# Kernel tuning notes

Measured on AMD Instinct MI355X. Metric: run time of the kernel, lower is better.

Reference implementation:

```python
import jax, jax.numpy as jnp
import numpy as np

K = 4
EPS = 1e-6
NEG_INF = -1e9


def _extract_patches(x, k):
    # x: [C, H, W] -> [P, C*k*k], P = (H-k+1)*(W-k+1), p = hp*Wp + wp
    C, H, W = x.shape
    Hp, Wp = H - k + 1, W - k + 1
    cols = jnp.stack([x[:, di:di + Hp, dj:dj + Wp]
                      for di in range(k) for dj in range(k)], axis=1)  # [C, k*k, Hp, Wp]
    return cols.reshape(C * k * k, Hp * Wp).T  # [P, C*k*k]


def setup_inputs() -> dict:
    key = jax.random.key(0)
    k1, k2, k3 = jax.random.split(key, 3)
    C, H, W = 32, 80, 80
    low = jax.random.normal(k1, (1, C, H, W), dtype=jnp.float32)
    high = jax.random.normal(k2, (1, C, H, W), dtype=jnp.float32)
    mask = jax.random.randint(k3, (H + 1, W + 1), 0, 2, dtype=jnp.int32)
    return {"low_level_features": low, "hight_level_features": high, "mask": mask}


def reference(low_level_features, hight_level_features, mask):
    k = K
    low = low_level_features[0]    # [C, H, W]
    high = hight_level_features[0]
    C, H, W = low.shape
    Hp, Wp = H - k + 1, W - k + 1
    P = Hp * Wp

    low_p = _extract_patches(low, k)    # [P, D], D = C*k*k (candidate patches)
    high_p = _extract_patches(high, k)  # [P, D] (query filters)
    norms = jnp.sqrt(jnp.sum(low_p * low_p, axis=1))  # torch.norm per patch, [P]

    # all-pairs cosine-distance scores: [P_query, P_candidate]
    scores = jnp.einsum('qd,pd->qp', high_p, low_p) / (norms + EPS)[None, :]
    # candidates where mask==1 (top-left of patch) are excluded (set to inf=-1e9)
    excl = (mask[:Hp, :Wp].reshape(-1) == 1)
    scores = jnp.where(excl[None, :], NEG_INF, scores)
    best = jnp.argmax(scores, axis=1)   # [P] best match per query patch

    # a query patch at (i,j) is processed only if its 4 mask corners are nonzero
    valid = ((mask[:Hp, :Wp] != 0) & (mask[:Hp, k:k + Wp] != 0) &
             (mask[k:k + Hp, :Wp] != 0) & (mask[k:k + Hp, k:k + Wp] != 0))
    validf = valid.astype(low.dtype).reshape(-1)  # [P]

    gathered = low_p[best] * validf[:, None]            # [P, D]
    g = gathered.reshape(Hp, Wp, C, k, k)               # per-query result patches
    vmap2d = validf.reshape(Hp, Wp)

    result = jnp.zeros_like(low)
    counts = jnp.zeros((H, W), low.dtype)
    for di in range(k):
        for dj in range(k):
            result = result.at[:, di:di + Hp, dj:dj + Wp].add(
                jnp.moveaxis(g[:, :, :, di, dj], -1, 0))
            counts = counts.at[di:di + Hp, dj:dj + Wp].add(vmap2d)

    out = result / (counts + EPS)[None, :, :]
    nz = counts != 0
    out = out * nz[None, :, :] + low * (~nz)[None, :, :]
    return out[None]  # [1, C, H, W]
```

## Files before the change

kernel.cpp:

```cpp
#include <hip/hip_runtime.h>
#include <hip/hip_bf16.h>

#define CC    32
#define HH    80
#define WW    80
#define HW    6400
#define HPQ   77
#define WPQ   77
#define PP    5929
#define DD    512
#define MSTR  81
#define NTILE 93
#define QTILES 372
#define NEGINF (-1e9f)

typedef __attribute__((ext_vector_type(4))) float f32x4;
typedef __attribute__((ext_vector_type(8))) short bf16x8;
typedef __attribute__((ext_vector_type(8))) unsigned short u16x8;

__device__ __forceinline__ void split_bf16(float v, unsigned short& hi, unsigned short& lo) {
    __hip_bfloat16 h = __float2bfloat16(v);
    float hf = __bfloat162float(h);
    __hip_bfloat16 lw = __float2bfloat16(v - hf);
    hi = *reinterpret_cast<unsigned short*>(&h);
    lo = *reinterpret_cast<unsigned short*>(&lw);
}

__global__ __launch_bounds__(256) void k_flags(const float* __restrict__ low,
                                               const int* __restrict__ mask,
                                               float* __restrict__ invn,
                                               int* __restrict__ excl,
                                               int* __restrict__ qslot,
                                               int* __restrict__ qlist,
                                               int* __restrict__ nvalid) {
    __shared__ float part[4][64];
    const int tid = threadIdx.x;
    const int pl = tid & 63;
    const int sl = tid >> 6;
    const int p = blockIdx.x * 64 + pl;

    float s = 0.f;
    if (p < PP) {
        int pi = p / WPQ, pj = p % WPQ;
        int base = pi * WW + pj;
        for (int c = sl * 8; c < sl * 8 + 8; ++c) {
            int b2 = c * HW + base;
#pragma unroll
            for (int di = 0; di < 4; ++di)
#pragma unroll
                for (int dj = 0; dj < 4; ++dj) {
                    float v = low[b2 + di * WW + dj];
                    s += v * v;
                }
        }
    }
    part[sl][pl] = s;
    __syncthreads();
    if (tid < 64 && p < PP) {
        float t = part[0][tid] + part[1][tid] + part[2][tid] + part[3][tid];
        invn[p] = 1.0f / (sqrtf(t) + 1e-6f);
        int pi = p / WPQ, pj = p % WPQ;
        int m00 = mask[pi * MSTR + pj];
        int m01 = mask[pi * MSTR + pj + 4];
        int m10 = mask[(pi + 4) * MSTR + pj];
        int m11 = mask[(pi + 4) * MSTR + pj + 4];
        excl[p] = (m00 == 1) ? 1 : 0;
        int v = (m00 != 0 && m01 != 0 && m10 != 0 && m11 != 0) ? 1 : 0;
        int slot = -1;
        if (v) {
            slot = atomicAdd(nvalid, 1);
            qlist[slot] = p;
        }
        qslot[p] = slot;
    }
}

__global__ __launch_bounds__(256) void k_pack(const float* __restrict__ low,
                                              const float* __restrict__ high,
                                              const float* __restrict__ invn,
                                              const int* __restrict__ qlist,
                                              const int* __restrict__ nvalid,
                                              unsigned short* __restrict__ Bhi,
                                              unsigned short* __restrict__ Blo,
                                              unsigned short* __restrict__ Ahi,
                                              unsigned short* __restrict__ Alo) {
    const int g = blockIdx.x;
    if (g < QTILES * 4) {
        int t = g * 256 + threadIdx.x;
        int l = t & 63;
        int s = (t >> 6) & 15;
        int u = t >> 10;
        int n = l & 15, quad = l >> 4;
        int p = u * 16 + n;
        int kbase = s * 32 + quad * 8;
        u16x8 vh, vl;
        if (p < PP) {
            float sc = invn[p];
            int pi = p / WPQ, pj = p % WPQ;
            int base = (kbase >> 4) * HW + pi * WW + pj;
#pragma unroll
            for (int j = 0; j < 8; ++j) {
                int kk = kbase + j;
                int di = (kk >> 2) & 3, dj = kk & 3;
                float v = low[base + di * WW + dj] * sc;
                unsigned short h, lo;
                split_bf16(v, h, lo);
                vh[j] = h; vl[j] = lo;
            }
        } else {
#pragma unroll
            for (int j = 0; j < 8; ++j) { vh[j] = 0; vl[j] = 0; }
        }
        int off = t * 8;
        *reinterpret_cast<u16x8*>(Bhi + off) = vh;
        *reinterpret_cast<u16x8*>(Blo + off) = vl;
    } else {
        int t = (g - QTILES * 4) * 256 + threadIdx.x;
        int nv = *nvalid;
        int l = t & 63;
        int s = (t >> 6) & 15;
        int u = t >> 10;
        if ((u >> 2) * 64 >= nv) return;
        int m = l & 15, quad = l >> 4;
        int slot = u * 16 + m;
        int kbase = s * 32 + quad * 8;
        u16x8 vh, vl;
        if (slot < nv) {
            int q = qlist[slot];
            int qi = q / WPQ, qj = q % WPQ;
            int base = (kbase >> 4) * HW + qi * WW + qj;
#pragma unroll
            for (int j = 0; j < 8; ++j) {
                int kk = kbase + j;
                int di = (kk >> 2) & 3, dj = kk & 3;
                float v = high[base + di * WW + dj];
                unsigned short h, lo;
                split_bf16(v, h, lo);
                vh[j] = h; vl[j] = lo;
            }
        } else {
#pragma unroll
            for (int j = 0; j < 8; ++j) { vh[j] = 0; vl[j] = 0; }
        }
        int off = t * 8;
        *reinterpret_cast<u16x8*>(Ahi + off) = vh;
        *reinterpret_cast<u16x8*>(Alo + off) = vl;
    }
}

__global__ __launch_bounds__(256) void k_score(const unsigned short* __restrict__ Ahi,
                                               const unsigned short* __restrict__ Alo,
                                               const unsigned short* __restrict__ Bhi,
                                               const unsigned short* __restrict__ Blo,
                                               const int* __restrict__ excl,
                                               const int* __restrict__ nvalid,
                                               unsigned long long* __restrict__ bestpk) {
    const int nv = *nvalid;
    const int w = threadIdx.x >> 6;
    const int l = threadIdx.x & 63;
    const int pblk = blockIdx.x * 4 + w;
    const int n = l & 15, quad = l >> 4;
    const int bbase = pblk * 4 * 8192 + l * 8;

    int gpv[4]; bool exv[4];
#pragma unroll
    for (int pt = 0; pt < 4; ++pt) {
        gpv[pt] = pblk * 64 + pt * 16 + n;
        exv[pt] = (gpv[pt] < PP) ? (excl[gpv[pt]] != 0) : true;
    }

    for (int qblk = blockIdx.y; qblk * 64 < nv; qblk += 12) {
        f32x4 acc[4][4];
#pragma unroll
        for (int qt = 0; qt < 4; ++qt)
#pragma unroll
            for (int pt = 0; pt < 4; ++pt) acc[qt][pt] = (f32x4){0.f, 0.f, 0.f, 0.f};

        const int abase = qblk * 4 * 8192 + l * 8;
#pragma unroll 2
        for (int s = 0; s < 16; ++s) {
            bf16x8 ah[4], al[4];
#pragma unroll
            for (int qt = 0; qt < 4; ++qt) {
                ah[qt] = *reinterpret_cast<const bf16x8*>(Ahi + abase + qt * 8192 + s * 512);
                al[qt] = *reinterpret_cast<const bf16x8*>(Alo + abase + qt * 8192 + s * 512);
            }
#pragma unroll
            for (int pt = 0; pt < 4; ++pt) {
                bf16x8 bh = *reinterpret_cast<const bf16x8*>(Bhi + bbase + pt * 8192 + s * 512);
                bf16x8 bl = *reinterpret_cast<const bf16x8*>(Blo + bbase + pt * 8192 + s * 512);
#pragma unroll
                for (int qt = 0; qt < 4; ++qt) {
                    acc[qt][pt] = __builtin_amdgcn_mfma_f32_16x16x32_bf16(ah[qt], bh, acc[qt][pt], 0, 0, 0);
                    acc[qt][pt] = __builtin_amdgcn_mfma_f32_16x16x32_bf16(ah[qt], bl, acc[qt][pt], 0, 0, 0);
                    acc[qt][pt] = __builtin_amdgcn_mfma_f32_16x16x32_bf16(al[qt], bh, acc[qt][pt], 0, 0, 0);
                }
            }
        }

#pragma unroll
        for (int qt = 0; qt < 4; ++qt) {
            float bs[4]; int bi[4];
#pragma unroll
            for (int r = 0; r < 4; ++r) { bs[r] = -3.4e38f; bi[r] = 0x7fffffff; }
#pragma unroll
            for (int pt = 0; pt < 4; ++pt) {
                if (gpv[pt] < PP) {
#pragma unroll
                    for (int r = 0; r < 4; ++r) {
                        float sv = exv[pt] ? NEGINF : acc[qt][pt][r];
                        if (sv > bs[r]) { bs[r] = sv; bi[r] = gpv[pt]; }
                    }
                }
            }
#pragma unroll
            for (int off = 1; off <= 8; off <<= 1) {
#pragma unroll
                for (int r = 0; r < 4; ++r) {
                    float s2 = __shfl_xor(bs[r], off, 64);
                    int   i2 = __shfl_xor(bi[r], off, 64);
                    if (s2 > bs[r] || (s2 == bs[r] && i2 < bi[r])) { bs[r] = s2; bi[r] = i2; }
                }
            }
            if (n == 0) {
#pragma unroll
                for (int r = 0; r < 4; ++r) {
                    if (bi[r] != 0x7fffffff) {
                        unsigned ub = __float_as_uint(bs[r]);
                        unsigned mo = (ub & 0x80000000u) ? ~ub : (ub | 0x80000000u);
                        unsigned long long pk =
                            ((unsigned long long)mo << 32) | (unsigned)(~bi[r]);
                        int slot = (qblk * 4 + qt) * 16 + quad * 4 + r;
                        atomicMax(bestpk + slot, pk);
                    }
                }
            }
        }
    }
}

__global__ __launch_bounds__(256) void k_out(const float* __restrict__ low,
                                             const int* __restrict__ qslot,
                                             const unsigned long long* __restrict__ bestpk,
                                             float* __restrict__ out) {
    __shared__ int scnt[64];
    __shared__ int soff[64][17];
    const int tid = threadIdx.x;
    const int pixb = blockIdx.x * 64;
    if (tid < 64) {
        int pix = pixb + tid;
        int i = pix / WW, j = pix % WW;
        int nn = 0;
#pragma unroll
        for (int di = 0; di < 4; ++di) {
            int qi = i - di;
            if (qi < 0 || qi >= HPQ) continue;
#pragma unroll
            for (int dj = 0; dj < 4; ++dj) {
                int qj = j - dj;
                if (qj < 0 || qj >= WPQ) continue;
                int sl = qslot[qi * WPQ + qj];
                if (sl >= 0) {
                    int b = (int)(~(unsigned)bestpk[sl]);
                    soff[tid][nn++] = (b / WPQ + di) * WW + (b % WPQ + dj);
                }
            }
        }
        scnt[tid] = nn;
    }
    __syncthreads();
    const int pl = tid & 63, cg = tid >> 6;
    const int nn = scnt[pl];
    const int pix = pixb + pl;
    const float inv = 1.0f / ((float)nn + 1e-6f);
#pragma unroll
    for (int k = 0; k < 8; ++k) {
        int c = cg * 8 + k;
        int base = c * HW;
        float a;
        if (nn > 0) {
            a = 0.f;
            for (int t2 = 0; t2 < nn; ++t2) a += low[base + soff[pl][t2]];
            a *= inv;
        } else {
            a = low[base + pix];
        }
        out[base + pix] = a;
    }
}

extern "C" void kernel_launch(void* const* d_in, const int* in_sizes, int n_in,
                              void* d_out, int out_size, void* d_ws, size_t ws_size,
                              hipStream_t stream) {
    const float* low  = (const float*)d_in[0];
    const float* high = (const float*)d_in[1];
    const int*   mask = (const int*)d_in[2];
    float* out = (float*)d_out;

    char* ws = (char*)d_ws;
    int* nvalid = (int*)ws;
    unsigned long long* bestpk = (unsigned long long*)(ws + 64);
    int*   qlist = (int*)(ws + 49216);
    int*   qslot = (int*)(ws + 73024);
    float* invn  = (float*)(ws + 96832);
    int*   excl  = (int*)(ws + 120640);
    unsigned short* Ahi = (unsigned short*)(ws + 144448);
    unsigned short* Alo = (unsigned short*)(ws + 6239296);
    unsigned short* Bhi = (unsigned short*)(ws + 12334144);
    unsigned short* Blo = (unsigned short*)(ws + 18625600);

    hipMemsetAsync(ws, 0, 49216, stream);
    hipLaunchKernelGGL(k_flags, dim3(NTILE), dim3(256), 0, stream,
                       low, mask, invn, excl, qslot, qlist, nvalid);
    hipLaunchKernelGGL(k_pack, dim3(QTILES * 8), dim3(256), 0, stream,
                       low, high, invn, qlist, nvalid, Bhi, Blo, Ahi, Alo);
    hipLaunchKernelGGL(k_score, dim3(24, 12), dim3(256), 0, stream,
                       Ahi, Alo, Bhi, Blo, excl, nvalid, bestpk);
    hipLaunchKernelGGL(k_out, dim3(100), dim3(256), 0, stream,
                       low, qslot, bestpk, out);
}
```

Measured before the change: 114.2 us.

## Fuse flag and pack kernels, apply norm scale in epilogue, retile score grid

Merges the flag/norm kernel with the packing kernel into one launch. The candidate norm scaling moves out of B packing and into the score epilogue, and each flag block packs its own valid query patches straight into their atomically assigned slots. The score kernel is retiled so each wave handles one query tile against a block's 64 candidates, with a grid of 93x12 instead of 24x12. This removes a launch and a dependency bubble and increases parallelism in scoring. In exchange, each wave reuses B fragments less, and the scale is applied after the hi/lo split rather than before it, which slightly changes the rounding.

```diff
diff --git a/kernel.cpp b/kernel.cpp
--- a/kernel.cpp
+++ b/kernel.cpp
@@ -26,67 +26,22 @@
     lo = *reinterpret_cast<unsigned short*>(&lw);
 }
 
-__global__ __launch_bounds__(256) void k_flags(const float* __restrict__ low,
-                                               const int* __restrict__ mask,
-                                               float* __restrict__ invn,
-                                               int* __restrict__ excl,
-                                               int* __restrict__ qslot,
-                                               int* __restrict__ qlist,
-                                               int* __restrict__ nvalid) {
-    __shared__ float part[4][64];
-    const int tid = threadIdx.x;
-    const int pl = tid & 63;
-    const int sl = tid >> 6;
-    const int p = blockIdx.x * 64 + pl;
-
-    float s = 0.f;
-    if (p < PP) {
-        int pi = p / WPQ, pj = p % WPQ;
-        int base = pi * WW + pj;
-        for (int c = sl * 8; c < sl * 8 + 8; ++c) {
-            int b2 = c * HW + base;
-#pragma unroll
-            for (int di = 0; di < 4; ++di)
-#pragma unroll
-                for (int dj = 0; dj < 4; ++dj) {
-                    float v = low[b2 + di * WW + dj];
-                    s += v * v;
-                }
-        }
-    }
-    part[sl][pl] = s;
-    __syncthreads();
-    if (tid < 64 && p < PP) {
-        float t = part[0][tid] + part[1][tid] + part[2][tid] + part[3][tid];
-        invn[p] = 1.0f / (sqrtf(t) + 1e-6f);
-        int pi = p / WPQ, pj = p % WPQ;
-        int m00 = mask[pi * MSTR + pj];
-        int m01 = mask[pi * MSTR + pj + 4];
-        int m10 = mask[(pi + 4) * MSTR + pj];
-        int m11 = mask[(pi + 4) * MSTR + pj + 4];
-        excl[p] = (m00 == 1) ? 1 : 0;
-        int v = (m00 != 0 && m01 != 0 && m10 != 0 && m11 != 0) ? 1 : 0;
-        int slot = -1;
-        if (v) {
-            slot = atomicAdd(nvalid, 1);
-            qlist[slot] = p;
-        }
-        qslot[p] = slot;
-    }
-}
-
-__global__ __launch_bounds__(256) void k_pack(const float* __restrict__ low,
+__global__ __launch_bounds__(256) void k_main(const float* __restrict__ low,
                                               const float* __restrict__ high,
-                                              const float* __restrict__ invn,
-                                              const int* __restrict__ qlist,
-                                              const int* __restrict__ nvalid,
+                                              const int* __restrict__ mask,
+                                              float* __restrict__ invn,
+                                              int* __restrict__ excl,
+                                              int* __restrict__ qslot,
+                                              int* __restrict__ nvalid,
                                               unsigned short* __restrict__ Bhi,
                                               unsigned short* __restrict__ Blo,
                                               unsigned short* __restrict__ Ahi,
                                               unsigned short* __restrict__ Alo) {
     const int g = blockIdx.x;
-    if (g < QTILES * 4) {
-        int t = g * 256 + threadIdx.x;
+    const int tid = threadIdx.x;
+
+    if (g >= NTILE) {
+        int t = (g - NTILE) * 256 + tid;
         int l = t & 63;
         int s = (t >> 6) & 15;
         int u = t >> 10;
@@ -95,16 +50,14 @@
         int kbase = s * 32 + quad * 8;
         u16x8 vh, vl;
         if (p < PP) {
-            float sc = invn[p];
             int pi = p / WPQ, pj = p % WPQ;
             int base = (kbase >> 4) * HW + pi * WW + pj;
 #pragma unroll
             for (int j = 0; j < 8; ++j) {
                 int kk = kbase + j;
                 int di = (kk >> 2) & 3, dj = kk & 3;
-                float v = low[base + di * WW + dj] * sc;
                 unsigned short h, lo;
-                split_bf16(v, h, lo);
+                split_bf16(low[base + di * WW + dj], h, lo);
                 vh[j] = h; vl[j] = lo;
             }
         } else {
@@ -114,35 +67,74 @@
         int off = t * 8;
         *reinterpret_cast<u16x8*>(Bhi + off) = vh;
         *reinterpret_cast<u16x8*>(Blo + off) = vl;
-    } else {
-        int t = (g - QTILES * 4) * 256 + threadIdx.x;
-        int nv = *nvalid;
-        int l = t & 63;
-        int s = (t >> 6) & 15;
-        int u = t >> 10;
-        if ((u >> 2) * 64 >= nv) return;
-        int m = l & 15, quad = l >> 4;
-        int slot = u * 16 + m;
-        int kbase = s * 32 + quad * 8;
+        return;
+    }
+
+    __shared__ float part[4][64];
+    __shared__ int s_n;
+    __shared__ int s_q[64];
+    __shared__ int s_slot[64];
+    const int pl = tid & 63;
+    const int slc = tid >> 6;
+    const int p = g * 64 + pl;
+
+    float s = 0.f;
+    if (p < PP) {
+        int pi = p / WPQ, pj = p % WPQ;
+        int base = pi * WW + pj;
+        for (int c = slc * 8; c < slc * 8 + 8; ++c) {
+            int b2 = c * HW + base;
+#pragma unroll
+            for (int di = 0; di < 4; ++di)
+#pragma unroll
+                for (int dj = 0; dj < 4; ++dj) {
+                    float v = low[b2 + di * WW + dj];
+                    s += v * v;
+                }
+        }
+    }
+    part[slc][pl] = s;
+    if (tid == 0) s_n = 0;
+    __syncthreads();
+    if (tid < 64 && p < PP) {
+        float t4 = part[0][tid] + part[1][tid] + part[2][tid] + part[3][tid];
+        invn[p] = 1.0f / (sqrtf(t4) + 1e-6f);
+        int pi = p / WPQ, pj = p % WPQ;
+        int m00 = mask[pi * MSTR + pj];
+        int m01 = mask[pi * MSTR + pj + 4];
+        int m10 = mask[(pi + 4) * MSTR + pj];
+        int m11 = mask[(pi + 4) * MSTR + pj + 4];
+        excl[p] = (m00 == 1) ? 1 : 0;
+        int slot = -1;
+        if (m00 != 0 && m01 != 0 && m10 != 0 && m11 != 0) {
+            slot = atomicAdd(nvalid, 1);
+            int li = atomicAdd(&s_n, 1);
+            s_q[li] = p;
+            s_slot[li] = slot;
+        }
+        qslot[p] = slot;
+    }
+    __syncthreads();
+
+    const int nn = s_n;
+    const int c64 = tid & 63;
+    const int ss = c64 >> 2, qd = c64 & 3;
+    const int kbase = ss * 32 + qd * 8;
+    for (int vi = tid >> 6; vi < nn; vi += 4) {
+        int q = s_q[vi], slot = s_slot[vi];
+        int qi = q / WPQ, qj = q % WPQ;
+        int base = (kbase >> 4) * HW + qi * WW + qj;
         u16x8 vh, vl;
-        if (slot < nv) {
-            int q = qlist[slot];
-            int qi = q / WPQ, qj = q % WPQ;
-            int base = (kbase >> 4) * HW + qi * WW + qj;
-#pragma unroll
-            for (int j = 0; j < 8; ++j) {
-                int kk = kbase + j;
-                int di = (kk >> 2) & 3, dj = kk & 3;
-                float v = high[base + di * WW + dj];
-                unsigned short h, lo;
-                split_bf16(v, h, lo);
-                vh[j] = h; vl[j] = lo;
-            }
-        } else {
-#pragma unroll
-            for (int j = 0; j < 8; ++j) { vh[j] = 0; vl[j] = 0; }
-        }
-        int off = t * 8;
+#pragma unroll
+        for (int j = 0; j < 8; ++j) {
+            int kk = kbase + j;
+            int di = (kk >> 2) & 3, dj = kk & 3;
+            unsigned short h, lo;
+            split_bf16(high[base + di * WW + dj], h, lo);
+            vh[j] = h; vl[j] = lo;
+        }
+        int u = slot >> 4, m = slot & 15;
+        int off = u * 8192 + ss * 512 + (qd * 16 + m) * 8;
         *reinterpret_cast<u16x8*>(Ahi + off) = vh;
         *reinterpret_cast<u16x8*>(Alo + off) = vl;
     }
@@ -153,86 +145,77 @@
                                                const unsigned short* __restrict__ Bhi,
                                                const unsigned short* __restrict__ Blo,
                                                const int* __restrict__ excl,
+                                               const float* __restrict__ invn,
                                                const int* __restrict__ nvalid,
                                                unsigned long long* __restrict__ bestpk) {
     const int nv = *nvalid;
     const int w = threadIdx.x >> 6;
     const int l = threadIdx.x & 63;
-    const int pblk = blockIdx.x * 4 + w;
+    const int pblk = blockIdx.x;
     const int n = l & 15, quad = l >> 4;
     const int bbase = pblk * 4 * 8192 + l * 8;
 
-    int gpv[4]; bool exv[4];
+    int gpv[4]; bool exv[4]; float ivv[4];
 #pragma unroll
     for (int pt = 0; pt < 4; ++pt) {
         gpv[pt] = pblk * 64 + pt * 16 + n;
-        exv[pt] = (gpv[pt] < PP) ? (excl[gpv[pt]] != 0) : true;
+        if (gpv[pt] < PP) { exv[pt] = (excl[gpv[pt]] != 0); ivv[pt] = invn[gpv[pt]]; }
+        else              { exv[pt] = true;                 ivv[pt] = 0.f; }
     }
 
     for (int qblk = blockIdx.y; qblk * 64 < nv; qblk += 12) {
-        f32x4 acc[4][4];
-#pragma unroll
-        for (int qt = 0; qt < 4; ++qt)
-#pragma unroll
-            for (int pt = 0; pt < 4; ++pt) acc[qt][pt] = (f32x4){0.f, 0.f, 0.f, 0.f};
-
-        const int abase = qblk * 4 * 8192 + l * 8;
-#pragma unroll 2
+        const int qtile = qblk * 4 + w;
+        f32x4 acc[4];
+#pragma unroll
+        for (int pt = 0; pt < 4; ++pt) acc[pt] = (f32x4){0.f, 0.f, 0.f, 0.f};
+
+        const int abase = qtile * 8192 + l * 8;
+#pragma unroll 4
         for (int s = 0; s < 16; ++s) {
-            bf16x8 ah[4], al[4];
-#pragma unroll
-            for (int qt = 0; qt < 4; ++qt) {
-                ah[qt] = *reinterpret_cast<const bf16x8*>(Ahi + abase + qt * 8192 + s * 512);
-                al[qt] = *reinterpret_cast<const bf16x8*>(Alo + abase + qt * 8192 + s * 512);
-            }
+            bf16x8 ah = *reinterpret_cast<const bf16x8*>(Ahi + abase + s * 512);
+            bf16x8 al = *reinterpret_cast<const bf16x8*>(Alo + abase + s * 512);
 #pragma unroll
             for (int pt = 0; pt < 4; ++pt) {
                 bf16x8 bh = *reinterpret_cast<const bf16x8*>(Bhi + bbase + pt * 8192 + s * 512);
                 bf16x8 bl = *reinterpret_cast<const bf16x8*>(Blo + bbase + pt * 8192 + s * 512);
-#pragma unroll
-                for (int qt = 0; qt < 4; ++qt) {
-                    acc[qt][pt] = __builtin_amdgcn_mfma_f32_16x16x32_bf16(ah[qt], bh, acc[qt][pt], 0, 0, 0);
-                    acc[qt][pt] = __builtin_amdgcn_mfma_f32_16x16x32_bf16(ah[qt], bl, acc[qt][pt], 0, 0, 0);
-                    acc[qt][pt] = __builtin_amdgcn_mfma_f32_16x16x32_bf16(al[qt], bh, acc[qt][pt], 0, 0, 0);
+                acc[pt] = __builtin_amdgcn_mfma_f32_16x16x32_bf16(ah, bh, acc[pt], 0, 0, 0);
+                acc[pt] = __builtin_amdgcn_mfma_f32_16x16x32_bf16(ah, bl, acc[pt], 0, 0, 0);
+                acc[pt] = __builtin_amdgcn_mfma_f32_16x16x32_bf16(al, bh, acc[pt], 0, 0, 0);
+            }
+        }
+
+        float bs[4]; int bi[4];
+#pragma unroll
+        for (int r = 0; r < 4; ++r) { bs[r] = -3.4e38f; bi[r] = 0x7fffffff; }
+#pragma unroll
+        for (int pt = 0; pt < 4; ++pt) {
+            if (gpv[pt] < PP) {
+#pragma unroll
+                for (int r = 0; r < 4; ++r) {
+                    float sv = exv[pt] ? NEGINF : acc[pt][r] * ivv[pt];
+                    if (sv > bs[r]) { bs[r] = sv; bi[r] = gpv[pt]; }
                 }
             }
         }
-
-#pragma unroll
-        for (int qt = 0; qt < 4; ++qt) {
-            float bs[4]; int bi[4];
-#pragma unroll
-            for (int r = 0; r < 4; ++r) { bs[r] = -3.4e38f; bi[r] = 0x7fffffff; }
-#pragma unroll
-            for (int pt = 0; pt < 4; ++pt) {
-                if (gpv[pt] < PP) {
-#pragma unroll
-                    for (int r = 0; r < 4; ++r) {
-                        float sv = exv[pt] ? NEGINF : acc[qt][pt][r];
-                        if (sv > bs[r]) { bs[r] = sv; bi[r] = gpv[pt]; }
-                    }
-                }
-            }
-#pragma unroll
-            for (int off = 1; off <= 8; off <<= 1) {
-#pragma unroll
-                for (int r = 0; r < 4; ++r) {
-                    float s2 = __shfl_xor(bs[r], off, 64);
-                    int   i2 = __shfl_xor(bi[r], off, 64);
-                    if (s2 > bs[r] || (s2 == bs[r] && i2 < bi[r])) { bs[r] = s2; bi[r] = i2; }
-                }
-            }
-            if (n == 0) {
-#pragma unroll
-                for (int r = 0; r < 4; ++r) {
-                    if (bi[r] != 0x7fffffff) {
-                        unsigned ub = __float_as_uint(bs[r]);
-                        unsigned mo = (ub & 0x80000000u) ? ~ub : (ub | 0x80000000u);
-                        unsigned long long pk =
-                            ((unsigned long long)mo << 32) | (unsigned)(~bi[r]);
-                        int slot = (qblk * 4 + qt) * 16 + quad * 4 + r;
-                        atomicMax(bestpk + slot, pk);
-                    }
+#pragma unroll
+        for (int off = 1; off <= 8; off <<= 1) {
+#pragma unroll
+            for (int r = 0; r < 4; ++r) {
+                float s2 = __shfl_xor(bs[r], off, 64);
+                int   i2 = __shfl_xor(bi[r], off, 64);
+                if (s2 > bs[r] || (s2 == bs[r] && i2 < bi[r])) { bs[r] = s2; bi[r] = i2; }
+            }
+        }
+        if (n == 0) {
+#pragma unroll
+            for (int r = 0; r < 4; ++r) {
+                if (bi[r] != 0x7fffffff) {
+                    unsigned ub = __float_as_uint(bs[r]);
+                    unsigned mo = (ub & 0x80000000u) ? ~ub : (ub | 0x80000000u);
+                    unsigned long long pk =
+                        ((unsigned long long)mo << 32) | (unsigned)(~bi[r]);
+                    int slot = qtile * 16 + quad * 4 + r;
+                    atomicMax(bestpk + slot, pk);
                 }
             }
         }
@@ -300,22 +283,19 @@
     char* ws = (char*)d_ws;
     int* nvalid = (int*)ws;
     unsigned long long* bestpk = (unsigned long long*)(ws + 64);
-    int*   qlist = (int*)(ws + 49216);
-    int*   qslot = (int*)(ws + 73024);
-    float* invn  = (float*)(ws + 96832);
-    int*   excl  = (int*)(ws + 120640);
-    unsigned short* Ahi = (unsigned short*)(ws + 144448);
-    unsigned short* Alo = (unsigned short*)(ws + 6239296);
-    unsigned short* Bhi = (unsigned short*)(ws + 12334144);
-    unsigned short* Blo = (unsigned short*)(ws + 18625600);
+    int*   qslot = (int*)(ws + 49216);
+    float* invn  = (float*)(ws + 73024);
+    int*   excl  = (int*)(ws + 96832);
+    unsigned short* Ahi = (unsigned short*)(ws + 120640);
+    unsigned short* Alo = (unsigned short*)(ws + 6215488);
+    unsigned short* Bhi = (unsigned short*)(ws + 12310336);
+    unsigned short* Blo = (unsigned short*)(ws + 18405184);
 
     hipMemsetAsync(ws, 0, 49216, stream);
-    hipLaunchKernelGGL(k_flags, dim3(NTILE), dim3(256), 0, stream,
-                       low, mask, invn, excl, qslot, qlist, nvalid);
-    hipLaunchKernelGGL(k_pack, dim3(QTILES * 8), dim3(256), 0, stream,
-                       low, high, invn, qlist, nvalid, Bhi, Blo, Ahi, Alo);
-    hipLaunchKernelGGL(k_score, dim3(24, 12), dim3(256), 0, stream,
-                       Ahi, Alo, Bhi, Blo, excl, nvalid, bestpk);
+    hipLaunchKernelGGL(k_main, dim3(NTILE + QTILES * 4), dim3(256), 0, stream,
+                       low, high, mask, invn, excl, qslot, nvalid, Bhi, Blo, Ahi, Alo);
+    hipLaunchKernelGGL(k_score, dim3(NTILE, 12), dim3(256), 0, stream,
+                       Ahi, Alo, Bhi, Blo, excl, invn, nvalid, bestpk);
     hipLaunchKernelGGL(k_out, dim3(100), dim3(256), 0, stream,
                        low, qslot, bestpk, out);
 }
```

Result: slower. 120.0 us (+5.0%).
